# Kernel tuning notes

Measured on AMD Instinct MI355X. Metric: run time of the kernel, lower is better.

Reference implementation:

```python
import jax, jax.numpy as jnp
import numpy as np
from jax import lax

_SOBEL_X = jnp.array([[-1., 0., 1.], [-2., 0., 2.], [-1., 0., 1.]], dtype=jnp.float32)
_SOBEL_Y = jnp.array([[1., 2., 1.], [0., 0., 0.], [-1., -2., -1.]], dtype=jnp.float32)


def rgb2ycrcb(x):
    # x: [B,3,H,W] -> [B,3,H,W] (Y, Cr, Cb)
    R, G, B = x[:, 0], x[:, 1], x[:, 2]
    Y = 0.299 * R + 0.587 * G + 0.114 * B
    Cr = (R - Y) * 0.713 + 0.5
    Cb = (B - Y) * 0.564 + 0.5
    return jnp.stack([Y, Cr, Cb], axis=1)


def depthwise_sobel(x):
    # x: [B,3,H,W]; per-channel 3x3 cross-correlation with SAME padding (matches F.conv2d pad=1)
    C = x.shape[1]
    wx = jnp.broadcast_to(_SOBEL_X[None, None], (C, 1, 3, 3))
    wy = jnp.broadcast_to(_SOBEL_Y[None, None], (C, 1, 3, 3))
    dn = ('NCHW', 'OIHW', 'NCHW')
    gx = lax.conv_general_dilated(x, wx, (1, 1), 'SAME', feature_group_count=C, dimension_numbers=dn)
    gy = lax.conv_general_dilated(x, wy, (1, 1), 'SAME', feature_group_count=C, dimension_numbers=dn)
    return gx, gy


def adjust_gamma(img, gamma, gain=1.0):
    # torchvision float path: clamp(gain * img**gamma, 0, 1)
    return jnp.clip(gain * img ** gamma, 0.0, 1.0)


def adjust_contrast(img, factor):
    # torchvision: blend with per-image mean of grayscale, then clamp
    gray = 0.2989 * img[:, 0:1] + 0.587 * img[:, 1:2] + 0.114 * img[:, 2:3]
    mean = jnp.mean(gray, axis=(1, 2, 3), keepdims=True)
    return jnp.clip(factor * img + (1.0 - factor) * mean, 0.0, 1.0)


def l1(a, b):
    return jnp.mean(jnp.abs(a - b))


def fusion_loss(input_vis, input_ir, output, Mask):
    Fuse = output * Mask
    ycc_fuse = rgb2ycrcb(Fuse)
    Cr_F, Cb_F = ycc_fuse[:, 1:2], ycc_fuse[:, 2:3]

    R_vis = adjust_gamma(input_vis, 0.5, 1.0)
    ycc_vis = rgb2ycrcb(R_vis)
    Cr_V, Cb_V = ycc_vis[:, 1:2], ycc_vis[:, 2:3]

    R_ir = adjust_contrast(input_ir, 1.8)

    fgx, fgy = depthwise_sobel(Fuse)
    vgx, vgy = depthwise_sobel(R_vis)
    igx, igy = depthwise_sobel(R_ir)

    joint_gx = jnp.maximum(vgx, igx)
    joint_gy = jnp.maximum(vgy, igy)
    joint_int = jnp.maximum(R_vis, R_ir)

    con_loss = l1(Fuse, joint_int)
    grad_loss = 0.5 * l1(fgx, joint_gx) + 0.5 * l1(fgy, joint_gy)
    color_loss = l1(Cb_F, Cb_V) + l1(Cr_F, Cr_V)
    return 0.5 * con_loss + 0.2 * grad_loss + 1.0 * color_loss


def setup_inputs() -> dict:
    key = jax.random.key(0)
    k1, k2, k3, k4 = jax.random.split(key, 4)
    B, C, H, W = 16, 3, 512, 512
    return {
        'input_vis': jax.random.uniform(k1, (B, C, H, W), dtype=jnp.float32),
        'input_ir': jax.random.uniform(k2, (B, C, H, W), dtype=jnp.float32),
        'output': jax.random.uniform(k3, (B, C, H, W), dtype=jnp.float32),
        'Mask': jax.random.uniform(k4, (B, C, H, W), dtype=jnp.float32),
    }


def reference(input_vis, input_ir, output, Mask):
    return fusion_loss(input_vis, input_ir, output, Mask)
```

## Files before the change

kernel.cpp:

```cpp
#include <hip/hip_runtime.h>
#include <math.h>

#define Bn 16
#define Cn 3
#define Hn 512
#define Wn 512
#define HWn (Hn*Wn)
#define CHWn (Cn*HWn)
#define Rr 8

__device__ __forceinline__ float clamp01(float x) {
    return fminf(fmaxf(x, 0.0f), 1.0f);
}

__global__ __launch_bounds__(256) void gray_mean_kernel(
        const float* __restrict__ ir, float* __restrict__ ws)
{
    const int b = blockIdx.y;
    const int tid = threadIdx.x;
    const float* base = ir + (size_t)b * CHWn;

    float sr = 0.f, sg = 0.f, sb = 0.f;
#pragma unroll
    for (int k = 0; k < 8; ++k) {
        size_t px = (size_t)blockIdx.x * 8192 + (size_t)(k * 256 + tid) * 4;
        float4 r4 = *(const float4*)(base + px);
        float4 g4 = *(const float4*)(base + HWn + px);
        float4 b4 = *(const float4*)(base + 2 * HWn + px);
        sr += (r4.x + r4.y) + (r4.z + r4.w);
        sg += (g4.x + g4.y) + (g4.z + g4.w);
        sb += (b4.x + b4.y) + (b4.z + b4.w);
    }
    float s = 0.2989f * sr + 0.587f * sg + 0.114f * sb;

#pragma unroll
    for (int off = 32; off; off >>= 1) s += __shfl_down(s, off, 64);

    __shared__ float red[4];
    if ((tid & 63) == 0) red[tid >> 6] = s;
    __syncthreads();
    if (tid == 0) atomicAdd(&ws[b], (red[0] + red[1]) + (red[2] + red[3]));
}

__global__ __launch_bounds__(256) void fusion_main_kernel(
        const float* __restrict__ vis, const float* __restrict__ ir,
        const float* __restrict__ outp, const float* __restrict__ mask,
        float* __restrict__ ws)
{
    const int tid = threadIdx.x;
    const int tx = tid & 127;
    const int sy = tid >> 7;
    const int b  = blockIdx.y;
    const int y0 = (blockIdx.x * 2 + sy) * Rr;
    const int x0 = tx * 4;

    const float mean_b = ws[b] * (1.0f / (float)HWn);
    const float moff = 0.8f * mean_b;

    const size_t bb = (size_t)b * CHWn;
    const float* pv = vis  + bb;
    const float* pi = ir   + bb;
    const float* po = outp + bb;
    const float* pm = mask + bb;

    float conA = 0.f, gxA = 0.f, gyA = 0.f;

    for (int c = 0; c < 3; ++c) {
        const float* v_ = pv + (size_t)c * HWn;
        const float* i_ = pi + (size_t)c * HWn;
        const float* o_ = po + (size_t)c * HWn;
        const float* m_ = pm + (size_t)c * HWn;

        float wf[3][6], wv[3][6], wi[3][6];

        auto load_row = [&](int y, int s) {
            if ((unsigned)y < (unsigned)Hn) {
                size_t o = (size_t)y * Wn + x0;
                float4 o4 = *(const float4*)(o_ + o);
                float4 m4 = *(const float4*)(m_ + o);
                float4 v4 = *(const float4*)(v_ + o);
                float4 i4 = *(const float4*)(i_ + o);
                float oL = 0.f, mL = 0.f, vL = 0.f, iL = 0.f;
                float oR = 0.f, mR = 0.f, vR = 0.f, iR = 0.f;
                if (x0 > 0)      { oL = o_[o - 1]; mL = m_[o - 1]; vL = v_[o - 1]; iL = i_[o - 1]; }
                if (x0 + 4 < Wn) { oR = o_[o + 4]; mR = m_[o + 4]; vR = v_[o + 4]; iR = i_[o + 4]; }

                wf[s][0] = oL * mL;     wf[s][1] = o4.x * m4.x;
                wf[s][2] = o4.y * m4.y; wf[s][3] = o4.z * m4.z;
                wf[s][4] = o4.w * m4.w; wf[s][5] = oR * mR;

                wv[s][0] = clamp01(sqrtf(vL));   wv[s][1] = clamp01(sqrtf(v4.x));
                wv[s][2] = clamp01(sqrtf(v4.y)); wv[s][3] = clamp01(sqrtf(v4.z));
                wv[s][4] = clamp01(sqrtf(v4.w)); wv[s][5] = clamp01(sqrtf(vR));

                wi[s][0] = clamp01(fmaf(1.8f, iL,   -moff));
                wi[s][1] = clamp01(fmaf(1.8f, i4.x, -moff));
                wi[s][2] = clamp01(fmaf(1.8f, i4.y, -moff));
                wi[s][3] = clamp01(fmaf(1.8f, i4.z, -moff));
                wi[s][4] = clamp01(fmaf(1.8f, i4.w, -moff));
                wi[s][5] = clamp01(fmaf(1.8f, iR,   -moff));
                if (x0 == 0)       { wf[s][0] = 0.f; wv[s][0] = 0.f; wi[s][0] = 0.f; }
                if (x0 + 4 >= Wn)  { wf[s][5] = 0.f; wv[s][5] = 0.f; wi[s][5] = 0.f; }
            } else {
#pragma unroll
                for (int k = 0; k < 6; ++k) { wf[s][k] = 0.f; wv[s][k] = 0.f; wi[s][k] = 0.f; }
            }
        };

        load_row(y0 - 1, 0);
        load_row(y0,     1);

        for (int yy = 0; yy < Rr; ++yy) {
            load_row(y0 + yy + 1, 2);

#pragma unroll
            for (int j = 0; j < 4; ++j) {
                float gxf = (wf[0][j+2] - wf[0][j]) + 2.f * (wf[1][j+2] - wf[1][j]) + (wf[2][j+2] - wf[2][j]);
                float gyf = (wf[0][j] + 2.f * wf[0][j+1] + wf[0][j+2]) - (wf[2][j] + 2.f * wf[2][j+1] + wf[2][j+2]);

                float gxv = (wv[0][j+2] - wv[0][j]) + 2.f * (wv[1][j+2] - wv[1][j]) + (wv[2][j+2] - wv[2][j]);
                float gyv = (wv[0][j] + 2.f * wv[0][j+1] + wv[0][j+2]) - (wv[2][j] + 2.f * wv[2][j+1] + wv[2][j+2]);

                float gxi = (wi[0][j+2] - wi[0][j]) + 2.f * (wi[1][j+2] - wi[1][j]) + (wi[2][j+2] - wi[2][j]);
                float gyi = (wi[0][j] + 2.f * wi[0][j+1] + wi[0][j+2]) - (wi[2][j] + 2.f * wi[2][j+1] + wi[2][j+2]);

                gxA  += fabsf(gxf - fmaxf(gxv, gxi));
                gyA  += fabsf(gyf - fmaxf(gyv, gyi));
                conA += fabsf(wf[1][j+1] - fmaxf(wv[1][j+1], wi[1][j+1]));
            }

#pragma unroll
            for (int k = 0; k < 6; ++k) {
                wf[0][k] = wf[1][k]; wf[1][k] = wf[2][k];
                wv[0][k] = wv[1][k]; wv[1][k] = wv[2][k];
                wi[0][k] = wi[1][k]; wi[1][k] = wi[2][k];
            }
        }
    }

    float crA = 0.f, cbA = 0.f;
    {
        auto px = [&](float fr, float fg, float fb, float vr, float vg, float vb) {
            float fY = 0.299f * fr + 0.587f * fg + 0.114f * fb;
            float vY = 0.299f * vr + 0.587f * vg + 0.114f * vb;
            float crf = (fr - fY) * 0.713f, crv = (vr - vY) * 0.713f;
            float cbf = (fb - fY) * 0.564f, cbv = (vb - vY) * 0.564f;
            crA += fabsf(crf - crv);
            cbA += fabsf(cbf - cbv);
        };
        for (int y = y0; y < y0 + Rr; ++y) {
            size_t o = (size_t)y * Wn + x0;
            float4 oR = *(const float4*)(po + o);
            float4 oG = *(const float4*)(po + HWn + o);
            float4 oB = *(const float4*)(po + 2 * HWn + o);
            float4 mR = *(const float4*)(pm + o);
            float4 mG = *(const float4*)(pm + HWn + o);
            float4 mB = *(const float4*)(pm + 2 * HWn + o);
            float4 vR = *(const float4*)(pv + o);
            float4 vG = *(const float4*)(pv + HWn + o);
            float4 vB = *(const float4*)(pv + 2 * HWn + o);
            px(oR.x * mR.x, oG.x * mG.x, oB.x * mB.x,
               clamp01(sqrtf(vR.x)), clamp01(sqrtf(vG.x)), clamp01(sqrtf(vB.x)));
            px(oR.y * mR.y, oG.y * mG.y, oB.y * mB.y,
               clamp01(sqrtf(vR.y)), clamp01(sqrtf(vG.y)), clamp01(sqrtf(vB.y)));
            px(oR.z * mR.z, oG.z * mG.z, oB.z * mB.z,
               clamp01(sqrtf(vR.z)), clamp01(sqrtf(vG.z)), clamp01(sqrtf(vB.z)));
            px(oR.w * mR.w, oG.w * mG.w, oB.w * mB.w,
               clamp01(sqrtf(vR.w)), clamp01(sqrtf(vG.w)), clamp01(sqrtf(vB.w)));
        }
    }

    auto wred = [](float x) {
#pragma unroll
        for (int off = 32; off; off >>= 1) x += __shfl_down(x, off, 64);
        return x;
    };
    conA = wred(conA); gxA = wred(gxA); gyA = wred(gyA);
    crA  = wred(crA);  cbA = wred(cbA);

    __shared__ float red[5][4];
    const int lane = tid & 63, w = tid >> 6;
    if (lane == 0) {
        red[0][w] = conA; red[1][w] = gxA; red[2][w] = gyA;
        red[3][w] = crA;  red[4][w] = cbA;
    }
    __syncthreads();
    if (tid < 5) {
        float s = (red[tid][0] + red[tid][1]) + (red[tid][2] + red[tid][3]);
        atomicAdd(&ws[16 + tid], s);
    }
}

__global__ void finalize_kernel(const float* __restrict__ ws, float* __restrict__ out)
{
    if (threadIdx.x == 0 && blockIdx.x == 0) {
        const float invN3 = 1.0f / (float)((size_t)Bn * Cn * HWn);
        const float invN1 = 1.0f / (float)((size_t)Bn * HWn);
        float con = ws[16] * invN3;
        float gx  = ws[17] * invN3;
        float gy  = ws[18] * invN3;
        float cr  = ws[19] * invN1;
        float cb  = ws[20] * invN1;
        out[0] = 0.5f * con + 0.2f * (0.5f * gx + 0.5f * gy) + (cb + cr);
    }
}

extern "C" void kernel_launch(void* const* d_in, const int* in_sizes, int n_in,
                              void* d_out, int out_size, void* d_ws, size_t ws_size,
                              hipStream_t stream)
{
    const float* vis = (const float*)d_in[0];
    const float* ir  = (const float*)d_in[1];
    const float* out = (const float*)d_in[2];
    const float* msk = (const float*)d_in[3];
    float* ws = (float*)d_ws;

    hipMemsetAsync(ws, 0, 32 * sizeof(float), stream);

    gray_mean_kernel<<<dim3(32, Bn), 256, 0, stream>>>(ir, ws);
    fusion_main_kernel<<<dim3(Hn / (2 * Rr), Bn), 256, 0, stream>>>(vis, ir, out, msk, ws);
    finalize_kernel<<<1, 64, 0, stream>>>(ws, (float*)d_out);
}
```

Measured before the change: 240.3 us.

## Use wavefront shuffles for halo columns and shrink per-thread row tiles

Each thread now gets its left and right neighbour columns from adjacent lanes through shuffles. Only the wavefront edge lanes still issue scalar global loads for the halo, which replaces four scalar loads per row per thread. Rows per thread drop from 8 to 2 and the gray-mean grid grows from 32 to 128 blocks per image, giving more blocks and more parallelism. The row loops are fully unrolled. The cost is a larger vertical halo reload fraction (4 loaded rows per 2 output rows) and more atomics.

Measured after the change: 248.7 us. 1.04x slower.

```diff
diff --git a/kernel.cpp b/kernel.cpp
--- a/kernel.cpp
+++ b/kernel.cpp
@@ -7,7 +7,7 @@
 #define Wn 512
 #define HWn (Hn*Wn)
 #define CHWn (Cn*HWn)
-#define Rr 8
+#define Rr 2
 
 __device__ __forceinline__ float clamp01(float x) {
     return fminf(fmaxf(x, 0.0f), 1.0f);
@@ -22,8 +22,8 @@
 
     float sr = 0.f, sg = 0.f, sb = 0.f;
 #pragma unroll
-    for (int k = 0; k < 8; ++k) {
-        size_t px = (size_t)blockIdx.x * 8192 + (size_t)(k * 256 + tid) * 4;
+    for (int k = 0; k < 2; ++k) {
+        size_t px = (size_t)blockIdx.x * 2048 + (size_t)(k * 256 + tid) * 4;
         float4 r4 = *(const float4*)(base + px);
         float4 g4 = *(const float4*)(base + HWn + px);
         float4 b4 = *(const float4*)(base + 2 * HWn + px);
@@ -47,12 +47,13 @@
         const float* __restrict__ outp, const float* __restrict__ mask,
         float* __restrict__ ws)
 {
-    const int tid = threadIdx.x;
-    const int tx = tid & 127;
-    const int sy = tid >> 7;
-    const int b  = blockIdx.y;
-    const int y0 = (blockIdx.x * 2 + sy) * Rr;
-    const int x0 = tx * 4;
+    const int tid  = threadIdx.x;
+    const int tx   = tid & 127;
+    const int sy   = tid >> 7;
+    const int lane = tid & 63;
+    const int b    = blockIdx.y;
+    const int y0   = (blockIdx.x * 2 + sy) * Rr;
+    const int x0   = tx * 4;
 
     const float mean_b = ws[b] * (1.0f / (float)HWn);
     const float moff = 0.8f * mean_b;
@@ -80,27 +81,52 @@
                 float4 m4 = *(const float4*)(m_ + o);
                 float4 v4 = *(const float4*)(v_ + o);
                 float4 i4 = *(const float4*)(i_ + o);
-                float oL = 0.f, mL = 0.f, vL = 0.f, iL = 0.f;
-                float oR = 0.f, mR = 0.f, vR = 0.f, iR = 0.f;
-                if (x0 > 0)      { oL = o_[o - 1]; mL = m_[o - 1]; vL = v_[o - 1]; iL = i_[o - 1]; }
-                if (x0 + 4 < Wn) { oR = o_[o + 4]; mR = m_[o + 4]; vR = v_[o + 4]; iR = i_[o + 4]; }
-
-                wf[s][0] = oL * mL;     wf[s][1] = o4.x * m4.x;
-                wf[s][2] = o4.y * m4.y; wf[s][3] = o4.z * m4.z;
-                wf[s][4] = o4.w * m4.w; wf[s][5] = oR * mR;
-
-                wv[s][0] = clamp01(sqrtf(vL));   wv[s][1] = clamp01(sqrtf(v4.x));
-                wv[s][2] = clamp01(sqrtf(v4.y)); wv[s][3] = clamp01(sqrtf(v4.z));
-                wv[s][4] = clamp01(sqrtf(v4.w)); wv[s][5] = clamp01(sqrtf(vR));
-
-                wi[s][0] = clamp01(fmaf(1.8f, iL,   -moff));
-                wi[s][1] = clamp01(fmaf(1.8f, i4.x, -moff));
-                wi[s][2] = clamp01(fmaf(1.8f, i4.y, -moff));
-                wi[s][3] = clamp01(fmaf(1.8f, i4.z, -moff));
-                wi[s][4] = clamp01(fmaf(1.8f, i4.w, -moff));
-                wi[s][5] = clamp01(fmaf(1.8f, iR,   -moff));
-                if (x0 == 0)       { wf[s][0] = 0.f; wv[s][0] = 0.f; wi[s][0] = 0.f; }
-                if (x0 + 4 >= Wn)  { wf[s][5] = 0.f; wv[s][5] = 0.f; wi[s][5] = 0.f; }
+
+                float df0 = o4.x * m4.x, df1 = o4.y * m4.y;
+                float df2 = o4.z * m4.z, df3 = o4.w * m4.w;
+                float dv0 = clamp01(sqrtf(v4.x)), dv1 = clamp01(sqrtf(v4.y));
+                float dv2 = clamp01(sqrtf(v4.z)), dv3 = clamp01(sqrtf(v4.w));
+                float di0 = clamp01(fmaf(1.8f, i4.x, -moff));
+                float di1 = clamp01(fmaf(1.8f, i4.y, -moff));
+                float di2 = clamp01(fmaf(1.8f, i4.z, -moff));
+                float di3 = clamp01(fmaf(1.8f, i4.w, -moff));
+
+                float lf = __shfl_up(df3, 1, 64);
+                float lv = __shfl_up(dv3, 1, 64);
+                float li = __shfl_up(di3, 1, 64);
+                float rf = __shfl_down(df0, 1, 64);
+                float rv = __shfl_down(dv0, 1, 64);
+                float ri = __shfl_down(di0, 1, 64);
+
+                if (lane == 0) {
+                    if (x0 > 0) {
+                        float ol = o_[o - 1], ml = m_[o - 1];
+                        float vl = v_[o - 1], il = i_[o - 1];
+                        lf = ol * ml;
+                        lv = clamp01(sqrtf(vl));
+                        li = clamp01(fmaf(1.8f, il, -moff));
+                    } else {
+                        lf = 0.f; lv = 0.f; li = 0.f;
+                    }
+                }
+                if (lane == 63) {
+                    if (x0 + 4 < Wn) {
+                        float orr = o_[o + 4], mr = m_[o + 4];
+                        float vr  = v_[o + 4], ir2 = i_[o + 4];
+                        rf = orr * mr;
+                        rv = clamp01(sqrtf(vr));
+                        ri = clamp01(fmaf(1.8f, ir2, -moff));
+                    } else {
+                        rf = 0.f; rv = 0.f; ri = 0.f;
+                    }
+                }
+
+                wf[s][0] = lf; wf[s][1] = df0; wf[s][2] = df1;
+                wf[s][3] = df2; wf[s][4] = df3; wf[s][5] = rf;
+                wv[s][0] = lv; wv[s][1] = dv0; wv[s][2] = dv1;
+                wv[s][3] = dv2; wv[s][4] = dv3; wv[s][5] = rv;
+                wi[s][0] = li; wi[s][1] = di0; wi[s][2] = di1;
+                wi[s][3] = di2; wi[s][4] = di3; wi[s][5] = ri;
             } else {
 #pragma unroll
                 for (int k = 0; k < 6; ++k) { wf[s][k] = 0.f; wv[s][k] = 0.f; wi[s][k] = 0.f; }
@@ -110,6 +136,7 @@
         load_row(y0 - 1, 0);
         load_row(y0,     1);
 
+#pragma unroll
         for (int yy = 0; yy < Rr; ++yy) {
             load_row(y0 + yy + 1, 2);
 
@@ -148,8 +175,9 @@
             crA += fabsf(crf - crv);
             cbA += fabsf(cbf - cbv);
         };
-        for (int y = y0; y < y0 + Rr; ++y) {
-            size_t o = (size_t)y * Wn + x0;
+#pragma unroll
+        for (int yy = 0; yy < Rr; ++yy) {
+            size_t o = (size_t)(y0 + yy) * Wn + x0;
             float4 oR = *(const float4*)(po + o);
             float4 oG = *(const float4*)(po + HWn + o);
             float4 oB = *(const float4*)(po + 2 * HWn + o);
@@ -179,7 +207,7 @@
     crA  = wred(crA);  cbA = wred(cbA);
 
     __shared__ float red[5][4];
-    const int lane = tid & 63, w = tid >> 6;
+    const int w = tid >> 6;
     if (lane == 0) {
         red[0][w] = conA; red[1][w] = gxA; red[2][w] = gyA;
         red[3][w] = crA;  red[4][w] = cbA;
@@ -217,7 +245,7 @@
 
     hipMemsetAsync(ws, 0, 32 * sizeof(float), stream);
 
-    gray_mean_kernel<<<dim3(32, Bn), 256, 0, stream>>>(ir, ws);
+    gray_mean_kernel<<<dim3(128, Bn), 256, 0, stream>>>(ir, ws);
     fusion_main_kernel<<<dim3(Hn / (2 * Rr), Bn), 256, 0, stream>>>(vis, ir, out, msk, ws);
     finalize_kernel<<<1, 64, 0, stream>>>(ws, (float*)d_out);
 }
```

## Use wavefront-per-row tiles with shuffle halos and more blocks

Applied to the files above, without the earlier changes.

Each wavefront now covers a full 512-wide row strip with 8 pixels per lane. The left and right halo values come from neighbouring lanes through shuffles instead of separate scalar global loads. The rolling three-row window uses modular indexing inside a fully unrolled loop, which removes the per-row register copies. Rows per thread drop from 8 to 4, and gray_mean uses four times as many blocks, so the grid is larger and better spread across CUs. The cost is more vertical halo reloads relative to useful rows and higher register pressure from the wider window.

Measured after the change: 257.0 us. 1.07x slower.

```diff
diff --git a/kernel.cpp b/kernel.cpp
--- a/kernel.cpp
+++ b/kernel.cpp
@@ -7,7 +7,7 @@
 #define Wn 512
 #define HWn (Hn*Wn)
 #define CHWn (Cn*HWn)
-#define Rr 8
+#define Rr 4
 
 __device__ __forceinline__ float clamp01(float x) {
     return fminf(fmaxf(x, 0.0f), 1.0f);
@@ -22,8 +22,8 @@
 
     float sr = 0.f, sg = 0.f, sb = 0.f;
 #pragma unroll
-    for (int k = 0; k < 8; ++k) {
-        size_t px = (size_t)blockIdx.x * 8192 + (size_t)(k * 256 + tid) * 4;
+    for (int k = 0; k < 2; ++k) {
+        size_t px = (size_t)blockIdx.x * 2048 + (size_t)(k * 256 + tid) * 4;
         float4 r4 = *(const float4*)(base + px);
         float4 g4 = *(const float4*)(base + HWn + px);
         float4 b4 = *(const float4*)(base + 2 * HWn + px);
@@ -42,17 +42,17 @@
     if (tid == 0) atomicAdd(&ws[b], (red[0] + red[1]) + (red[2] + red[3]));
 }
 
-__global__ __launch_bounds__(256) void fusion_main_kernel(
+__global__ __launch_bounds__(256, 2) void fusion_main_kernel(
         const float* __restrict__ vis, const float* __restrict__ ir,
         const float* __restrict__ outp, const float* __restrict__ mask,
         float* __restrict__ ws)
 {
-    const int tid = threadIdx.x;
-    const int tx = tid & 127;
-    const int sy = tid >> 7;
-    const int b  = blockIdx.y;
-    const int y0 = (blockIdx.x * 2 + sy) * Rr;
-    const int x0 = tx * 4;
+    const int tid  = threadIdx.x;
+    const int lane = tid & 63;
+    const int wv_id = tid >> 6;
+    const int b    = blockIdx.y;
+    const int y0   = (blockIdx.x * 4 + wv_id) * Rr;
+    const int x0   = lane * 8;
 
     const float mean_b = ws[b] * (1.0f / (float)HWn);
     const float moff = 0.8f * mean_b;
@@ -71,102 +71,135 @@
         const float* o_ = po + (size_t)c * HWn;
         const float* m_ = pm + (size_t)c * HWn;
 
-        float wf[3][6], wv[3][6], wi[3][6];
+        float wf[3][10], wvv[3][10], wi[3][10];
 
         auto load_row = [&](int y, int s) {
             if ((unsigned)y < (unsigned)Hn) {
                 size_t o = (size_t)y * Wn + x0;
-                float4 o4 = *(const float4*)(o_ + o);
-                float4 m4 = *(const float4*)(m_ + o);
-                float4 v4 = *(const float4*)(v_ + o);
-                float4 i4 = *(const float4*)(i_ + o);
-                float oL = 0.f, mL = 0.f, vL = 0.f, iL = 0.f;
-                float oR = 0.f, mR = 0.f, vR = 0.f, iR = 0.f;
-                if (x0 > 0)      { oL = o_[o - 1]; mL = m_[o - 1]; vL = v_[o - 1]; iL = i_[o - 1]; }
-                if (x0 + 4 < Wn) { oR = o_[o + 4]; mR = m_[o + 4]; vR = v_[o + 4]; iR = i_[o + 4]; }
-
-                wf[s][0] = oL * mL;     wf[s][1] = o4.x * m4.x;
-                wf[s][2] = o4.y * m4.y; wf[s][3] = o4.z * m4.z;
-                wf[s][4] = o4.w * m4.w; wf[s][5] = oR * mR;
-
-                wv[s][0] = clamp01(sqrtf(vL));   wv[s][1] = clamp01(sqrtf(v4.x));
-                wv[s][2] = clamp01(sqrtf(v4.y)); wv[s][3] = clamp01(sqrtf(v4.z));
-                wv[s][4] = clamp01(sqrtf(v4.w)); wv[s][5] = clamp01(sqrtf(vR));
-
-                wi[s][0] = clamp01(fmaf(1.8f, iL,   -moff));
-                wi[s][1] = clamp01(fmaf(1.8f, i4.x, -moff));
-                wi[s][2] = clamp01(fmaf(1.8f, i4.y, -moff));
-                wi[s][3] = clamp01(fmaf(1.8f, i4.z, -moff));
-                wi[s][4] = clamp01(fmaf(1.8f, i4.w, -moff));
-                wi[s][5] = clamp01(fmaf(1.8f, iR,   -moff));
-                if (x0 == 0)       { wf[s][0] = 0.f; wv[s][0] = 0.f; wi[s][0] = 0.f; }
-                if (x0 + 4 >= Wn)  { wf[s][5] = 0.f; wv[s][5] = 0.f; wi[s][5] = 0.f; }
+                float4 oa = *(const float4*)(o_ + o);
+                float4 ob = *(const float4*)(o_ + o + 4);
+                float4 ma = *(const float4*)(m_ + o);
+                float4 mb = *(const float4*)(m_ + o + 4);
+                float4 va = *(const float4*)(v_ + o);
+                float4 vb = *(const float4*)(v_ + o + 4);
+                float4 ia = *(const float4*)(i_ + o);
+                float4 ib = *(const float4*)(i_ + o + 4);
+
+                float df0 = oa.x * ma.x, df1 = oa.y * ma.y;
+                float df2 = oa.z * ma.z, df3 = oa.w * ma.w;
+                float df4 = ob.x * mb.x, df5 = ob.y * mb.y;
+                float df6 = ob.z * mb.z, df7 = ob.w * mb.w;
+
+                float dv0 = clamp01(sqrtf(va.x)), dv1 = clamp01(sqrtf(va.y));
+                float dv2 = clamp01(sqrtf(va.z)), dv3 = clamp01(sqrtf(va.w));
+                float dv4 = clamp01(sqrtf(vb.x)), dv5 = clamp01(sqrtf(vb.y));
+                float dv6 = clamp01(sqrtf(vb.z)), dv7 = clamp01(sqrtf(vb.w));
+
+                float di0 = clamp01(fmaf(1.8f, ia.x, -moff));
+                float di1 = clamp01(fmaf(1.8f, ia.y, -moff));
+                float di2 = clamp01(fmaf(1.8f, ia.z, -moff));
+                float di3 = clamp01(fmaf(1.8f, ia.w, -moff));
+                float di4 = clamp01(fmaf(1.8f, ib.x, -moff));
+                float di5 = clamp01(fmaf(1.8f, ib.y, -moff));
+                float di6 = clamp01(fmaf(1.8f, ib.z, -moff));
+                float di7 = clamp01(fmaf(1.8f, ib.w, -moff));
+
+                float lf = __shfl_up(df7, 1, 64);
+                float lv = __shfl_up(dv7, 1, 64);
+                float li = __shfl_up(di7, 1, 64);
+                float rf = __shfl_down(df0, 1, 64);
+                float rv = __shfl_down(dv0, 1, 64);
+                float ri = __shfl_down(di0, 1, 64);
+                lf = (lane == 0)  ? 0.f : lf;
+                lv = (lane == 0)  ? 0.f : lv;
+                li = (lane == 0)  ? 0.f : li;
+                rf = (lane == 63) ? 0.f : rf;
+                rv = (lane == 63) ? 0.f : rv;
+                ri = (lane == 63) ? 0.f : ri;
+
+                wf[s][0] = lf;  wf[s][1] = df0; wf[s][2] = df1; wf[s][3] = df2;
+                wf[s][4] = df3; wf[s][5] = df4; wf[s][6] = df5; wf[s][7] = df6;
+                wf[s][8] = df7; wf[s][9] = rf;
+                wvv[s][0] = lv;  wvv[s][1] = dv0; wvv[s][2] = dv1; wvv[s][3] = dv2;
+                wvv[s][4] = dv3; wvv[s][5] = dv4; wvv[s][6] = dv5; wvv[s][7] = dv6;
+                wvv[s][8] = dv7; wvv[s][9] = rv;
+                wi[s][0] = li;  wi[s][1] = di0; wi[s][2] = di1; wi[s][3] = di2;
+                wi[s][4] = di3; wi[s][5] = di4; wi[s][6] = di5; wi[s][7] = di6;
+                wi[s][8] = di7; wi[s][9] = ri;
             } else {
 #pragma unroll
-                for (int k = 0; k < 6; ++k) { wf[s][k] = 0.f; wv[s][k] = 0.f; wi[s][k] = 0.f; }
+                for (int k = 0; k < 10; ++k) { wf[s][k] = 0.f; wvv[s][k] = 0.f; wi[s][k] = 0.f; }
             }
         };
 
         load_row(y0 - 1, 0);
         load_row(y0,     1);
 
+#pragma unroll
         for (int yy = 0; yy < Rr; ++yy) {
-            load_row(y0 + yy + 1, 2);
-
-#pragma unroll
-            for (int j = 0; j < 4; ++j) {
-                float gxf = (wf[0][j+2] - wf[0][j]) + 2.f * (wf[1][j+2] - wf[1][j]) + (wf[2][j+2] - wf[2][j]);
-                float gyf = (wf[0][j] + 2.f * wf[0][j+1] + wf[0][j+2]) - (wf[2][j] + 2.f * wf[2][j+1] + wf[2][j+2]);
-
-                float gxv = (wv[0][j+2] - wv[0][j]) + 2.f * (wv[1][j+2] - wv[1][j]) + (wv[2][j+2] - wv[2][j]);
-                float gyv = (wv[0][j] + 2.f * wv[0][j+1] + wv[0][j+2]) - (wv[2][j] + 2.f * wv[2][j+1] + wv[2][j+2]);
-
-                float gxi = (wi[0][j+2] - wi[0][j]) + 2.f * (wi[1][j+2] - wi[1][j]) + (wi[2][j+2] - wi[2][j]);
-                float gyi = (wi[0][j] + 2.f * wi[0][j+1] + wi[0][j+2]) - (wi[2][j] + 2.f * wi[2][j+1] + wi[2][j+2]);
+            const int st = yy % 3;
+            const int sm = (yy + 1) % 3;
+            const int sb = (yy + 2) % 3;
+            load_row(y0 + yy + 1, sb);
+
+#pragma unroll
+            for (int j = 0; j < 8; ++j) {
+                float gxf = (wf[st][j+2] - wf[st][j]) + 2.f * (wf[sm][j+2] - wf[sm][j]) + (wf[sb][j+2] - wf[sb][j]);
+                float gyf = (wf[st][j] + 2.f * wf[st][j+1] + wf[st][j+2]) - (wf[sb][j] + 2.f * wf[sb][j+1] + wf[sb][j+2]);
+
+                float gxv = (wvv[st][j+2] - wvv[st][j]) + 2.f * (wvv[sm][j+2] - wvv[sm][j]) + (wvv[sb][j+2] - wvv[sb][j]);
+                float gyv = (wvv[st][j] + 2.f * wvv[st][j+1] + wvv[st][j+2]) - (wvv[sb][j] + 2.f * wvv[sb][j+1] + wvv[sb][j+2]);
+
+                float gxi = (wi[st][j+2] - wi[st][j]) + 2.f * (wi[sm][j+2] - wi[sm][j]) + (wi[sb][j+2] - wi[sb][j]);
+                float gyi = (wi[st][j] + 2.f * wi[st][j+1] + wi[st][j+2]) - (wi[sb][j] + 2.f * wi[sb][j+1] + wi[sb][j+2]);
 
                 gxA  += fabsf(gxf - fmaxf(gxv, gxi));
                 gyA  += fabsf(gyf - fmaxf(gyv, gyi));
-                conA += fabsf(wf[1][j+1] - fmaxf(wv[1][j+1], wi[1][j+1]));
-            }
-
-#pragma unroll
-            for (int k = 0; k < 6; ++k) {
-                wf[0][k] = wf[1][k]; wf[1][k] = wf[2][k];
-                wv[0][k] = wv[1][k]; wv[1][k] = wv[2][k];
-                wi[0][k] = wi[1][k]; wi[1][k] = wi[2][k];
+                conA += fabsf(wf[sm][j+1] - fmaxf(wvv[sm][j+1], wi[sm][j+1]));
             }
         }
     }
 
     float crA = 0.f, cbA = 0.f;
     {
-        auto px = [&](float fr, float fg, float fb, float vr, float vg, float vb) {
-            float fY = 0.299f * fr + 0.587f * fg + 0.114f * fb;
-            float vY = 0.299f * vr + 0.587f * vg + 0.114f * vb;
-            float crf = (fr - fY) * 0.713f, crv = (vr - vY) * 0.713f;
-            float cbf = (fb - fY) * 0.564f, cbv = (vb - vY) * 0.564f;
-            crA += fabsf(crf - crv);
-            cbA += fabsf(cbf - cbv);
+        auto px4 = [&](float4 fR, float4 fG, float4 fB,
+                       float4 vR, float4 vG, float4 vB) {
+            auto one = [&](float fr, float fg, float fb, float vr, float vg, float vb) {
+                float fY = 0.299f * fr + 0.587f * fg + 0.114f * fb;
+                float vY = 0.299f * vr + 0.587f * vg + 0.114f * vb;
+                crA += fabsf((fr - fY) - (vr - vY)) * 0.713f;
+                cbA += fabsf((fb - fY) - (vb - vY)) * 0.564f;
+            };
+            one(fR.x, fG.x, fB.x, vR.x, vG.x, vB.x);
+            one(fR.y, fG.y, fB.y, vR.y, vG.y, vB.y);
+            one(fR.z, fG.z, fB.z, vR.z, vG.z, vB.z);
+            one(fR.w, fG.w, fB.w, vR.w, vG.w, vB.w);
         };
-        for (int y = y0; y < y0 + Rr; ++y) {
-            size_t o = (size_t)y * Wn + x0;
-            float4 oR = *(const float4*)(po + o);
-            float4 oG = *(const float4*)(po + HWn + o);
-            float4 oB = *(const float4*)(po + 2 * HWn + o);
-            float4 mR = *(const float4*)(pm + o);
-            float4 mG = *(const float4*)(pm + HWn + o);
-            float4 mB = *(const float4*)(pm + 2 * HWn + o);
-            float4 vR = *(const float4*)(pv + o);
-            float4 vG = *(const float4*)(pv + HWn + o);
-            float4 vB = *(const float4*)(pv + 2 * HWn + o);
-            px(oR.x * mR.x, oG.x * mG.x, oB.x * mB.x,
-               clamp01(sqrtf(vR.x)), clamp01(sqrtf(vG.x)), clamp01(sqrtf(vB.x)));
-            px(oR.y * mR.y, oG.y * mG.y, oB.y * mB.y,
-               clamp01(sqrtf(vR.y)), clamp01(sqrtf(vG.y)), clamp01(sqrtf(vB.y)));
-            px(oR.z * mR.z, oG.z * mG.z, oB.z * mB.z,
-               clamp01(sqrtf(vR.z)), clamp01(sqrtf(vG.z)), clamp01(sqrtf(vB.z)));
-            px(oR.w * mR.w, oG.w * mG.w, oB.w * mB.w,
-               clamp01(sqrtf(vR.w)), clamp01(sqrtf(vG.w)), clamp01(sqrtf(vB.w)));
+#pragma unroll
+        for (int yy = 0; yy < Rr; ++yy) {
+#pragma unroll
+            for (int h = 0; h < 2; ++h) {
+                size_t o = (size_t)(y0 + yy) * Wn + x0 + 4 * h;
+                float4 oR = *(const float4*)(po + o);
+                float4 oG = *(const float4*)(po + HWn + o);
+                float4 oB = *(const float4*)(po + 2 * HWn + o);
+                float4 mR = *(const float4*)(pm + o);
+                float4 mG = *(const float4*)(pm + HWn + o);
+                float4 mB = *(const float4*)(pm + 2 * HWn + o);
+                float4 vR = *(const float4*)(pv + o);
+                float4 vG = *(const float4*)(pv + HWn + o);
+                float4 vB = *(const float4*)(pv + 2 * HWn + o);
+                float4 fR = make_float4(oR.x*mR.x, oR.y*mR.y, oR.z*mR.z, oR.w*mR.w);
+                float4 fG = make_float4(oG.x*mG.x, oG.y*mG.y, oG.z*mG.z, oG.w*mG.w);
+                float4 fB = make_float4(oB.x*mB.x, oB.y*mB.y, oB.z*mB.z, oB.w*mB.w);
+                float4 rV = make_float4(clamp01(sqrtf(vR.x)), clamp01(sqrtf(vR.y)),
+                                        clamp01(sqrtf(vR.z)), clamp01(sqrtf(vR.w)));
+                float4 gV = make_float4(clamp01(sqrtf(vG.x)), clamp01(sqrtf(vG.y)),
+                                        clamp01(sqrtf(vG.z)), clamp01(sqrtf(vG.w)));
+                float4 bV = make_float4(clamp01(sqrtf(vB.x)), clamp01(sqrtf(vB.y)),
+                                        clamp01(sqrtf(vB.z)), clamp01(sqrtf(vB.w)));
+                px4(fR, fG, fB, rV, gV, bV);
+            }
         }
     }
 
@@ -179,10 +212,9 @@
     crA  = wred(crA);  cbA = wred(cbA);
 
     __shared__ float red[5][4];
-    const int lane = tid & 63, w = tid >> 6;
     if (lane == 0) {
-        red[0][w] = conA; red[1][w] = gxA; red[2][w] = gyA;
-        red[3][w] = crA;  red[4][w] = cbA;
+        red[0][wv_id] = conA; red[1][wv_id] = gxA; red[2][wv_id] = gyA;
+        red[3][wv_id] = crA;  red[4][wv_id] = cbA;
     }
     __syncthreads();
     if (tid < 5) {
@@ -217,7 +249,7 @@
 
     hipMemsetAsync(ws, 0, 32 * sizeof(float), stream);
 
-    gray_mean_kernel<<<dim3(32, Bn), 256, 0, stream>>>(ir, ws);
-    fusion_main_kernel<<<dim3(Hn / (2 * Rr), Bn), 256, 0, stream>>>(vis, ir, out, msk, ws);
+    gray_mean_kernel<<<dim3(128, Bn), 256, 0, stream>>>(ir, ws);
+    fusion_main_kernel<<<dim3(Hn / (4 * Rr), Bn), 256, 0, stream>>>(vis, ir, out, msk, ws);
     finalize_kernel<<<1, 64, 0, stream>>>(ws, (float*)d_out);
 }
```
